# Kernel optimization log

Measured on AMD Instinct MI355X. Metric: run time of the kernel, lower is better.

The kernel has to match this reference:

```python
import jax, jax.numpy as jnp
import numpy as np

B = 16384
D = 64            # bottom_mlp_layers[-1] = embedding_dim
DENSE = 512
HIST = 50         # history length per row
C_CAMP = 1000     # num_collisions for campaign table (sqrt(1e6))
C_FEAT = 316      # num_collisions for 1e5-vocab tables
NQ_CAMP = 1000    # ceil(1e6/1000)
NQ_FEAT = 317     # ceil(1e5/316)
NFEAT = 7
N = NFEAT + 1 + 1 # sparse features + dense row
PROJ = 128


def setup_inputs() -> dict:
    key = jax.random.key(0)
    ks = jax.random.split(key, 20)
    inp = {
        'x': jax.random.normal(ks[0], (B, DENSE), jnp.float32),
        'hist_idx': jax.random.randint(ks[1], (B * HIST,), 0, 1000000),
        'hist_offsets': jnp.arange(B, dtype=jnp.int64) * HIST,
        'feat_idx': jax.random.randint(ks[2], (B, NFEAT), 0, 100000),
        # QR embedding tables (quotient, remainder)
        'Wq_c': jax.random.normal(ks[3], (NQ_CAMP, D), jnp.float32) * 0.05,
        'Wr_c': jax.random.normal(ks[4], (C_CAMP, D), jnp.float32) * 0.05,
        'Wq_f': jax.random.normal(ks[5], (NFEAT, NQ_FEAT, D), jnp.float32) * 0.05,
        'Wr_f': jax.random.normal(ks[6], (NFEAT, C_FEAT, D), jnp.float32) * 0.05,
        # bottom MLP: 512->512 relu 512->256 relu 256->64
        'W0': jax.random.normal(ks[7], (512, DENSE), jnp.float32) * 0.03,
        'b0': jnp.zeros((512,), jnp.float32),
        'W1': jax.random.normal(ks[8], (256, 512), jnp.float32) * 0.04,
        'b1': jnp.zeros((256,), jnp.float32),
        'W2': jax.random.normal(ks[9], (64, 256), jnp.float32) * 0.06,
        'b2': jnp.zeros((64,), jnp.float32),
        # projection: (D + (N^2-N)/2) -> PROJ ; 64 + 36 = 100
        'Wp': jax.random.normal(ks[10], (PROJ, D + (N * N - N) // 2), jnp.float32) * 0.1,
        'bp': jnp.zeros((PROJ,), jnp.float32),
    }
    return inp


def _forward(x, hist_idx, hist_offsets, feat_idx, Wq_c, Wr_c, Wq_f, Wr_f,
             W0, b0, W1, b1, W2, b2, Wp, bp):
    # bottom MLP
    h = jax.nn.relu(x @ W0.T + b0)
    h = jax.nn.relu(h @ W1.T + b1)
    dense = h @ W2.T + b2                                   # [B, D]

    # QR embedding bag (mode='mean', operation='mult') for history feature
    e = Wq_c[hist_idx // C_CAMP] * Wr_c[hist_idx % C_CAMP]  # [M, D]
    M = hist_idx.shape[0]
    seg = jnp.cumsum(jnp.zeros((M,), jnp.int32).at[hist_offsets].add(1)) - 1
    sums = jax.ops.segment_sum(e, seg, num_segments=B)      # [B, D]
    counts = jnp.diff(jnp.concatenate([hist_offsets, jnp.array([M], hist_offsets.dtype)]))
    hist_emb = sums / counts[:, None].astype(sums.dtype)

    # single-valued QR lookups (bag size 1 -> mean == lookup)
    t = jnp.arange(NFEAT)[None, :]
    fe = Wq_f[t, feat_idx // C_FEAT] * Wr_f[t, feat_idx % C_FEAT]  # [B, NFEAT, D]

    # pairwise dot interaction: upper triangle (offset=1) of T @ T^T
    T = jnp.concatenate([dense[:, None, :], hist_emb[:, None, :], fe], axis=1)  # [B, N, D]
    Z = jnp.einsum('bnd,bmd->bnm', T, T)
    row, col = np.triu_indices(N, k=1)
    Z_flat = Z[:, row, col]                                  # [B, (N^2-N)/2]

    combined = jnp.concatenate([dense, Z_flat], axis=1)
    return combined @ Wp.T + bp                              # [B, PROJ]


def reference(x, hist_idx, hist_offsets, feat_idx, Wq_c, Wr_c, Wq_f, Wr_f,
              W0, b0, W1, b1, W2, b2, Wp, bp):
    return _forward(x, hist_idx, hist_offsets, feat_idx, Wq_c, Wr_c, Wq_f, Wr_f,
                    W0, b0, W1, b1, W2, b2, Wp, bp)
```

## Files before the change

### kernel.cpp

```cpp
#include <hip/hip_runtime.h>
#include <hip/hip_bf16.h>
#include <stdint.h>

#define DENSE_D 512
#define HIDDEN1 512
#define HIDDEN2 256
#define EMB_D   64
#define NFEAT   7
#define NROWS   9
#define NPAIRS  36
#define COMB    100
#define KPROJ   128
#define PROJ    128
#define C_CAMP  1000
#define C_FEAT  316
#define NQ_FEAT 317
#define TROWS   16
#define HISTMAX 52

typedef __attribute__((ext_vector_type(8)))  __bf16 bf16x8;
typedef __attribute__((ext_vector_type(8)))  unsigned short ushort8;
typedef __attribute__((ext_vector_type(4)))  float  facc4;

#define GLD_LDS16(gp, lp) __builtin_amdgcn_global_load_lds( \
    (__attribute__((address_space(1))) void*)(gp), \
    (__attribute__((address_space(3))) void*)(lp), 16, 0, 0)

__device__ inline unsigned short f2bf(float f) {
    __hip_bfloat16 h = __float2bfloat16(f);
    return *reinterpret_cast<unsigned short*>(&h);
}
__device__ inline float blo(unsigned int u) { return __uint_as_float(u << 16); }
__device__ inline float bhi(unsigned int u) { return __uint_as_float(u & 0xffff0000u); }

template<int BM, int BN, int BK, int WM, int WN, bool RELU, bool A_F32>
__global__ __launch_bounds__(WM * WN * 64)
void gemm16(const void* __restrict__ Avoid,
            const unsigned short* __restrict__ W,
            const float* __restrict__ bias,
            unsigned short* __restrict__ Cout,
            int M, int N, int K)
{
    constexpr int THREADS = WM * WN * 64;
    constexpr int MREP    = BM / (WM * 16);
    constexpr int NREP    = BN / (WN * 16);
    constexpr int SUB     = BK / 32;
    constexpr int ACH     = BM * BK / 8;
    constexpr int BCH     = BN * BK / 8;

    __shared__ __align__(16) unsigned short Asm[BK / 8][BM][8];
    __shared__ __align__(16) unsigned short Bsm[BK / 8][BN][8];

    const int tid  = threadIdx.x;
    const int lane = tid & 63;
    const int wave = tid >> 6;
    const int wm   = wave / WN;
    const int wn   = wave % WN;
    const int row0 = blockIdx.x * BM;
    const int col0 = blockIdx.y * BN;
    const int fr   = lane & 15;
    const int fk   = lane >> 4;

    facc4 acc[MREP][NREP] = {};

    for (int k0 = 0; k0 < K; k0 += BK) {
        if (A_F32) {
            const float* Af = (const float*)Avoid;
            #pragma unroll
            for (int it = 0; it < ACH / THREADS; ++it) {
                const int p  = it * THREADS + tid;
                const int r  = p & (BM - 1);
                const int kc = p / BM;
                const float* src = Af + (size_t)(row0 + r) * K + k0 + kc * 8;
                const float4 v0 = *reinterpret_cast<const float4*>(src);
                const float4 v1 = *reinterpret_cast<const float4*>(src + 4);
                ushort8 cv;
                cv[0] = f2bf(v0.x); cv[1] = f2bf(v0.y);
                cv[2] = f2bf(v0.z); cv[3] = f2bf(v0.w);
                cv[4] = f2bf(v1.x); cv[5] = f2bf(v1.y);
                cv[6] = f2bf(v1.z); cv[7] = f2bf(v1.w);
                *reinterpret_cast<ushort8*>(
                    (unsigned short*)(&Asm[0][0][0]) + (size_t)p * 8) = cv;
            }
        } else {
            const unsigned short* Ab = (const unsigned short*)Avoid;
            #pragma unroll
            for (int it = 0; it < ACH / THREADS; ++it) {
                const int p  = it * THREADS + tid;
                const int r  = p & (BM - 1);
                const int kc = p / BM;
                GLD_LDS16(Ab + (size_t)(row0 + r) * K + k0 + kc * 8,
                          (&Asm[0][0][0]) + (size_t)p * 8);
            }
        }
        #pragma unroll
        for (int it = 0; it < BCH / THREADS; ++it) {
            const int p  = it * THREADS + tid;
            const int r  = p & (BN - 1);
            const int kc = p / BN;
            GLD_LDS16(W + (size_t)(col0 + r) * K + k0 + kc * 8,
                      (&Bsm[0][0][0]) + (size_t)p * 8);
        }
        __syncthreads();

        #pragma unroll
        for (int s = 0; s < SUB; ++s) {
            bf16x8 af[MREP], bw[NREP];
            #pragma unroll
            for (int m = 0; m < MREP; ++m)
                af[m] = *reinterpret_cast<const bf16x8*>(
                    &Asm[s * 4 + fk][wm * (MREP * 16) + m * 16 + fr][0]);
            #pragma unroll
            for (int n = 0; n < NREP; ++n)
                bw[n] = *reinterpret_cast<const bf16x8*>(
                    &Bsm[s * 4 + fk][wn * (NREP * 16) + n * 16 + fr][0]);
            #pragma unroll
            for (int m = 0; m < MREP; ++m)
                #pragma unroll
                for (int n = 0; n < NREP; ++n)
                    acc[m][n] = __builtin_amdgcn_mfma_f32_16x16x32_bf16(
                        af[m], bw[n], acc[m][n], 0, 0, 0);
        }
        __syncthreads();
    }

    #pragma unroll
    for (int n = 0; n < NREP; ++n) {
        const int col = col0 + wn * (NREP * 16) + n * 16 + fr;
        const float bv = bias[col];
        #pragma unroll
        for (int m = 0; m < MREP; ++m) {
            #pragma unroll
            for (int j = 0; j < 4; ++j) {
                const int row = row0 + wm * (MREP * 16) + m * 16 + fk * 4 + j;
                float v = acc[m][n][j] + bv;
                if (RELU) v = fmaxf(v, 0.f);
                Cout[(size_t)row * N + col] = f2bf(v);
            }
        }
    }
}

__device__ inline void cast_seg(const float* __restrict__ src,
                                unsigned short* __restrict__ dst,
                                int n4, int id, int stride)
{
    for (int i = id; i < n4; i += stride) {
        const float4 v = reinterpret_cast<const float4*>(src)[i];
        ushort4 o;
        o.x = f2bf(v.x); o.y = f2bf(v.y); o.z = f2bf(v.z); o.w = f2bf(v.w);
        reinterpret_cast<ushort4*>(dst)[i] = o;
    }
}

__global__ __launch_bounds__(256)
void prep_all(const float* __restrict__ W0, const float* __restrict__ W1,
              const float* __restrict__ W2, const float* __restrict__ Wp,
              const float* __restrict__ Wq_c, const float* __restrict__ Wr_c,
              const float* __restrict__ Wq_f, const float* __restrict__ Wr_f,
              unsigned short* w0b, unsigned short* w1b, unsigned short* w2b,
              unsigned short* wpb, unsigned short* qcb, unsigned short* rcb,
              unsigned short* qfb, unsigned short* rfb)
{
    const int id = blockIdx.x * blockDim.x + threadIdx.x;
    const int stride = gridDim.x * blockDim.x;
    cast_seg(W0,   w0b, HIDDEN1 * DENSE_D / 4,   id, stride);
    cast_seg(W1,   w1b, HIDDEN2 * HIDDEN1 / 4,   id, stride);
    cast_seg(W2,   w2b, EMB_D * HIDDEN2 / 4,     id, stride);
    cast_seg(Wq_c, qcb, C_CAMP * EMB_D / 4,      id, stride);
    cast_seg(Wr_c, rcb, C_CAMP * EMB_D / 4,      id, stride);
    cast_seg(Wq_f, qfb, NFEAT * NQ_FEAT * EMB_D / 4, id, stride);
    cast_seg(Wr_f, rfb, NFEAT * C_FEAT * EMB_D / 4,  id, stride);
    for (int i = id; i < PROJ * KPROJ; i += stride) {
        const int r = i >> 7, c = i & 127;
        wpb[i] = (c < COMB) ? f2bf(Wp[r * COMB + c]) : (unsigned short)0;
    }
}

__global__ __launch_bounds__(256)
void tail_fused(const unsigned short* __restrict__ h1b,
                const unsigned short* __restrict__ w2b,
                const float* __restrict__ b2,
                const int* __restrict__ hist_idx,
                const int* __restrict__ hist_off,
                const int* __restrict__ feat_idx,
                const unsigned short* __restrict__ qcb,
                const unsigned short* __restrict__ rcb,
                const unsigned short* __restrict__ qfb,
                const unsigned short* __restrict__ rfb,
                const unsigned short* __restrict__ wpb,
                const float* __restrict__ bp,
                float* __restrict__ out,
                int B, int Mtot)
{
    const int r0   = blockIdx.x * TROWS;
    const int t    = threadIdx.x;
    const int lane = t & 63;
    const int wave = t >> 6;
    const int fr   = lane & 15;
    const int fk   = lane >> 4;

    __shared__ __align__(16) unsigned short T[TROWS][NROWS][68];
    __shared__ __align__(16) unsigned short combs[TROWS][136];
    __shared__ int2 soff[TROWS][HISTMAX];

    {
        facc4 acc = {};
        const unsigned short* arow = h1b + (size_t)(r0 + fr) * HIDDEN2;
        const unsigned short* brow = w2b + (size_t)(wave * 16 + fr) * HIDDEN2;
        #pragma unroll
        for (int kw = 0; kw < 8; ++kw) {
            const bf16x8 af = *reinterpret_cast<const bf16x8*>(arow + kw * 32 + fk * 8);
            const bf16x8 bw = *reinterpret_cast<const bf16x8*>(brow + kw * 32 + fk * 8);
            acc = __builtin_amdgcn_mfma_f32_16x16x32_bf16(af, bw, acc, 0, 0, 0);
        }
        const int col = wave * 16 + fr;
        const float bv = b2[col];
        #pragma unroll
        for (int j = 0; j < 4; ++j) {
            const int row = fk * 4 + j;
            const unsigned short hv = f2bf(acc[j] + bv);
            T[row][0][col]  = hv;
            combs[row][col] = hv;
        }
    }

    for (int p = t; p < TROWS * 18; p += 256) {
        const int row = p / 18, c = p % 18;
        *reinterpret_cast<unsigned int*>(&combs[row][100 + c * 2]) = 0u;
    }

    {
        const int row = t >> 4;
        const int oc  = t & 15;
        const int br  = r0 + row;

        const int fbase = br * NFEAT;
        #pragma unroll
        for (int f = 0; f < NFEAT; ++f) {
            const int fi = feat_idx[fbase + f];
            const int q = fi / C_FEAT, r = fi - q * C_FEAT;
            const uint2 qv = *reinterpret_cast<const uint2*>(
                qfb + ((size_t)f * NQ_FEAT + q) * EMB_D + oc * 4);
            const uint2 rv = *reinterpret_cast<const uint2*>(
                rfb + ((size_t)f * C_FEAT + r) * EMB_D + oc * 4);
            union { ushort4 v; uint2 u; } pk;
            pk.v.x = f2bf(blo(qv.x) * blo(rv.x));
            pk.v.y = f2bf(bhi(qv.x) * bhi(rv.x));
            pk.v.z = f2bf(blo(qv.y) * blo(rv.y));
            pk.v.w = f2bf(bhi(qv.y) * bhi(rv.y));
            *reinterpret_cast<uint2*>(&T[row][2 + f][oc * 4]) = pk.u;
        }

        const int start = hist_off[br];
        const int end   = (br + 1 < B) ? hist_off[br + 1] : Mtot;
        const int cnt   = end - start;
        const int* hp = hist_idx + start;
        for (int i = oc; i < cnt; i += 16) {
            const int hi = hp[i];
            const int q = hi / C_CAMP;
            soff[row][i] = make_int2(q * EMB_D, (hi - q * C_CAMP) * EMB_D);
        }

        const unsigned short* qb = qcb + oc * 4;
        const unsigned short* rb = rcb + oc * 4;
        float a0 = 0.f, a1 = 0.f, a2 = 0.f, a3 = 0.f;
        #pragma unroll 2
        for (int i = 0; i < cnt; ++i) {
            const int2 o = soff[row][i];
            const uint2 qv = *reinterpret_cast<const uint2*>(qb + o.x);
            const uint2 rv = *reinterpret_cast<const uint2*>(rb + o.y);
            a0 += blo(qv.x) * blo(rv.x);
            a1 += bhi(qv.x) * bhi(rv.x);
            a2 += blo(qv.y) * blo(rv.y);
            a3 += bhi(qv.y) * bhi(rv.y);
        }
        const float inv = 1.f / (float)max(cnt, 1);
        union { ushort4 v; uint2 u; } pk;
        pk.v.x = f2bf(a0 * inv); pk.v.y = f2bf(a1 * inv);
        pk.v.z = f2bf(a2 * inv); pk.v.w = f2bf(a3 * inv);
        *reinterpret_cast<uint2*>(&T[row][1][oc * 4]) = pk.u;
    }
    __syncthreads();

    for (int p = t; p < NPAIRS * TROWS; p += 256) {
        const int row = p & (TROWS - 1);
        const int pr  = p / TROWS;
        int i = 0, rem = pr;
        while (rem >= (NROWS - 1) - i) { rem -= (NROWS - 1) - i; ++i; }
        const int j = i + 1 + rem;
        const unsigned short* ti = &T[row][i][0];
        const unsigned short* tj = &T[row][j][0];
        float s = 0.f;
        #pragma unroll
        for (int d = 0; d < EMB_D; d += 4) {
            const uint2 u = *reinterpret_cast<const uint2*>(ti + d);
            const uint2 v = *reinterpret_cast<const uint2*>(tj + d);
            s += blo(u.x) * blo(v.x) + bhi(u.x) * bhi(v.x)
               + blo(u.y) * blo(v.y) + bhi(u.y) * bhi(v.y);
        }
        combs[row][EMB_D + pr] = f2bf(s);
    }
    __syncthreads();

    {
        facc4 acc[2] = {};
        #pragma unroll
        for (int kw = 0; kw < 4; ++kw) {
            const bf16x8 af = *reinterpret_cast<const bf16x8*>(
                &combs[fr][kw * 32 + fk * 8]);
            #pragma unroll
            for (int n = 0; n < 2; ++n) {
                const bf16x8 bw = *reinterpret_cast<const bf16x8*>(
                    wpb + (size_t)(wave * 32 + n * 16 + fr) * KPROJ + kw * 32 + fk * 8);
                acc[n] = __builtin_amdgcn_mfma_f32_16x16x32_bf16(af, bw, acc[n], 0, 0, 0);
            }
        }
        #pragma unroll
        for (int n = 0; n < 2; ++n) {
            const int col = wave * 32 + n * 16 + fr;
            const float bv = bp[col];
            #pragma unroll
            for (int j = 0; j < 4; ++j) {
                const int row = fk * 4 + j;
                out[(size_t)(r0 + row) * PROJ + col] = acc[n][j] + bv;
            }
        }
    }
}

extern "C" void kernel_launch(void* const* d_in, const int* in_sizes, int n_in,
                              void* d_out, int out_size, void* d_ws, size_t ws_size,
                              hipStream_t stream)
{
    const float* x        = (const float*)d_in[0];
    const int*   hist_idx = (const int*)  d_in[1];
    const int*   hist_off = (const int*)  d_in[2];
    const int*   feat_idx = (const int*)  d_in[3];
    const float* Wq_c     = (const float*)d_in[4];
    const float* Wr_c     = (const float*)d_in[5];
    const float* Wq_f     = (const float*)d_in[6];
    const float* Wr_f     = (const float*)d_in[7];
    const float* W0       = (const float*)d_in[8];
    const float* b0       = (const float*)d_in[9];
    const float* W1       = (const float*)d_in[10];
    const float* b1       = (const float*)d_in[11];
    const float* W2       = (const float*)d_in[12];
    const float* b2       = (const float*)d_in[13];
    const float* Wp       = (const float*)d_in[14];
    const float* bp       = (const float*)d_in[15];

    const int M    = in_sizes[0] / DENSE_D;
    const int Mtot = in_sizes[1];

    char* w = (char*)d_ws;
    auto take = [&](size_t bytes) { char* p = w; w += (bytes + 255) & ~(size_t)255; return p; };
    unsigned short* w0b = (unsigned short*)take(HIDDEN1 * DENSE_D * 2);
    unsigned short* w1b = (unsigned short*)take(HIDDEN2 * HIDDEN1 * 2);
    unsigned short* w2b = (unsigned short*)take(EMB_D * HIDDEN2 * 2);
    unsigned short* wpb = (unsigned short*)take(PROJ * KPROJ * 2);
    unsigned short* qcb = (unsigned short*)take(C_CAMP * EMB_D * 2);
    unsigned short* rcb = (unsigned short*)take(C_CAMP * EMB_D * 2);
    unsigned short* qfb = (unsigned short*)take(NFEAT * NQ_FEAT * EMB_D * 2);
    unsigned short* rfb = (unsigned short*)take(NFEAT * C_FEAT * EMB_D * 2);
    unsigned short* h0b = (unsigned short*)take((size_t)M * HIDDEN1 * 2);
    unsigned short* h1b = (unsigned short*)take((size_t)M * HIDDEN2 * 2);

    prep_all<<<256, 256, 0, stream>>>(W0, W1, W2, Wp, Wq_c, Wr_c, Wq_f, Wr_f,
                                      w0b, w1b, w2b, wpb, qcb, rcb, qfb, rfb);

    gemm16<128, 128, 32, 2, 2, true, true>
        <<<dim3(M / 128, HIDDEN1 / 128), 256, 0, stream>>>(
        x, w0b, b0, h0b, M, HIDDEN1, DENSE_D);

    gemm16<64, 128, 64, 1, 4, true, false>
        <<<dim3(M / 64, HIDDEN2 / 128), 256, 0, stream>>>(
        h0b, w1b, b1, h1b, M, HIDDEN2, HIDDEN1);

    tail_fused<<<M / TROWS, 256, 0, stream>>>(
        h1b, w2b, b2, hist_idx, hist_off, feat_idx,
        qcb, rcb, qfb, rfb, wpb, bp, (float*)d_out, M, Mtot);
}
```

Before: 85.07 us.

## Drop weight-cast prep kernel; cast weights on the fly and widen tail kernel

Removes the separate prep_all kernel that converted all weights and embedding tables to bf16. The GEMMs now load fp32 weights and convert them during tiling, and the first GEMM also casts the campaign QR tables as a side task. The tail kernel reads fp32 W2, Wp and the feature tables directly. It also grows to 512 threads and splits the history-bag gather across two halves, whose partial sums are reduced through shared memory. This saves one launch and a pass over the weights, at the cost of repeated fp32 loads and conversions in every block and direct LDS stores in place of async global_load_lds for B tiles.

Result: slower. 104.0 us (+22.2%).

```diff
diff --git a/kernel.cpp b/kernel.cpp
--- a/kernel.cpp
+++ b/kernel.cpp
@@ -10,7 +10,6 @@
 #define NROWS   9
 #define NPAIRS  36
 #define COMB    100
-#define KPROJ   128
 #define PROJ    128
 #define C_CAMP  1000
 #define C_FEAT  316
@@ -33,13 +32,18 @@
 __device__ inline float blo(unsigned int u) { return __uint_as_float(u << 16); }
 __device__ inline float bhi(unsigned int u) { return __uint_as_float(u & 0xffff0000u); }
 
-template<int BM, int BN, int BK, int WM, int WN, bool RELU, bool A_F32>
+union bfr8 { bf16x8 v; ushort8 u; };
+
+template<int BM, int BN, int BK, int WM, int WN, bool RELU,
+         bool A_F32, bool B_F32, bool CAST>
 __global__ __launch_bounds__(WM * WN * 64)
 void gemm16(const void* __restrict__ Avoid,
-            const unsigned short* __restrict__ W,
+            const void* __restrict__ Wvoid,
             const float* __restrict__ bias,
             unsigned short* __restrict__ Cout,
-            int M, int N, int K)
+            int M, int N, int K,
+            const float* __restrict__ qc, const float* __restrict__ rc,
+            unsigned short* __restrict__ qcb, unsigned short* __restrict__ rcb)
 {
     constexpr int THREADS = WM * WN * 64;
     constexpr int MREP    = BM / (WM * 16);
@@ -60,6 +64,19 @@
     const int col0 = blockIdx.y * BN;
     const int fr   = lane & 15;
     const int fk   = lane >> 4;
+
+    if (CAST) {
+        constexpr int N4 = C_CAMP * EMB_D / 4;
+        const int gid = (blockIdx.y * gridDim.x + blockIdx.x) * THREADS + tid;
+        if (gid < 2 * N4) {
+            const bool second = gid >= N4;
+            const int i = second ? gid - N4 : gid;
+            const float4 v = reinterpret_cast<const float4*>(second ? rc : qc)[i];
+            ushort4 o;
+            o.x = f2bf(v.x); o.y = f2bf(v.y); o.z = f2bf(v.z); o.w = f2bf(v.w);
+            reinterpret_cast<ushort4*>(second ? rcb : qcb)[i] = o;
+        }
+    }
 
     facc4 acc[MREP][NREP] = {};
 
@@ -93,13 +110,34 @@
                           (&Asm[0][0][0]) + (size_t)p * 8);
             }
         }
-        #pragma unroll
-        for (int it = 0; it < BCH / THREADS; ++it) {
-            const int p  = it * THREADS + tid;
-            const int r  = p & (BN - 1);
-            const int kc = p / BN;
-            GLD_LDS16(W + (size_t)(col0 + r) * K + k0 + kc * 8,
-                      (&Bsm[0][0][0]) + (size_t)p * 8);
+        if (B_F32) {
+            const float* Wf = (const float*)Wvoid;
+            #pragma unroll
+            for (int it = 0; it < BCH / THREADS; ++it) {
+                const int p  = it * THREADS + tid;
+                const int r  = p & (BN - 1);
+                const int kc = p / BN;
+                const float* src = Wf + (size_t)(col0 + r) * K + k0 + kc * 8;
+                const float4 v0 = *reinterpret_cast<const float4*>(src);
+                const float4 v1 = *reinterpret_cast<const float4*>(src + 4);
+                ushort8 cv;
+                cv[0] = f2bf(v0.x); cv[1] = f2bf(v0.y);
+                cv[2] = f2bf(v0.z); cv[3] = f2bf(v0.w);
+                cv[4] = f2bf(v1.x); cv[5] = f2bf(v1.y);
+                cv[6] = f2bf(v1.z); cv[7] = f2bf(v1.w);
+                *reinterpret_cast<ushort8*>(
+                    (unsigned short*)(&Bsm[0][0][0]) + (size_t)p * 8) = cv;
+            }
+        } else {
+            const unsigned short* Wb = (const unsigned short*)Wvoid;
+            #pragma unroll
+            for (int it = 0; it < BCH / THREADS; ++it) {
+                const int p  = it * THREADS + tid;
+                const int r  = p & (BN - 1);
+                const int kc = p / BN;
+                GLD_LDS16(Wb + (size_t)(col0 + r) * K + k0 + kc * 8,
+                          (&Bsm[0][0][0]) + (size_t)p * 8);
+            }
         }
         __syncthreads();
 
@@ -141,54 +179,18 @@
     }
 }
 
-__device__ inline void cast_seg(const float* __restrict__ src,
-                                unsigned short* __restrict__ dst,
-                                int n4, int id, int stride)
-{
-    for (int i = id; i < n4; i += stride) {
-        const float4 v = reinterpret_cast<const float4*>(src)[i];
-        ushort4 o;
-        o.x = f2bf(v.x); o.y = f2bf(v.y); o.z = f2bf(v.z); o.w = f2bf(v.w);
-        reinterpret_cast<ushort4*>(dst)[i] = o;
-    }
-}
-
-__global__ __launch_bounds__(256)
-void prep_all(const float* __restrict__ W0, const float* __restrict__ W1,
-              const float* __restrict__ W2, const float* __restrict__ Wp,
-              const float* __restrict__ Wq_c, const float* __restrict__ Wr_c,
-              const float* __restrict__ Wq_f, const float* __restrict__ Wr_f,
-              unsigned short* w0b, unsigned short* w1b, unsigned short* w2b,
-              unsigned short* wpb, unsigned short* qcb, unsigned short* rcb,
-              unsigned short* qfb, unsigned short* rfb)
-{
-    const int id = blockIdx.x * blockDim.x + threadIdx.x;
-    const int stride = gridDim.x * blockDim.x;
-    cast_seg(W0,   w0b, HIDDEN1 * DENSE_D / 4,   id, stride);
-    cast_seg(W1,   w1b, HIDDEN2 * HIDDEN1 / 4,   id, stride);
-    cast_seg(W2,   w2b, EMB_D * HIDDEN2 / 4,     id, stride);
-    cast_seg(Wq_c, qcb, C_CAMP * EMB_D / 4,      id, stride);
-    cast_seg(Wr_c, rcb, C_CAMP * EMB_D / 4,      id, stride);
-    cast_seg(Wq_f, qfb, NFEAT * NQ_FEAT * EMB_D / 4, id, stride);
-    cast_seg(Wr_f, rfb, NFEAT * C_FEAT * EMB_D / 4,  id, stride);
-    for (int i = id; i < PROJ * KPROJ; i += stride) {
-        const int r = i >> 7, c = i & 127;
-        wpb[i] = (c < COMB) ? f2bf(Wp[r * COMB + c]) : (unsigned short)0;
-    }
-}
-
-__global__ __launch_bounds__(256)
+__global__ __launch_bounds__(512)
 void tail_fused(const unsigned short* __restrict__ h1b,
-                const unsigned short* __restrict__ w2b,
+                const float* __restrict__ W2,
                 const float* __restrict__ b2,
                 const int* __restrict__ hist_idx,
                 const int* __restrict__ hist_off,
                 const int* __restrict__ feat_idx,
                 const unsigned short* __restrict__ qcb,
                 const unsigned short* __restrict__ rcb,
-                const unsigned short* __restrict__ qfb,
-                const unsigned short* __restrict__ rfb,
-                const unsigned short* __restrict__ wpb,
+                const float* __restrict__ Wq_f,
+                const float* __restrict__ Wr_f,
+                const float* __restrict__ Wp,
                 const float* __restrict__ bp,
                 float* __restrict__ out,
                 int B, int Mtot)
@@ -202,17 +204,24 @@
 
     __shared__ __align__(16) unsigned short T[TROWS][NROWS][68];
     __shared__ __align__(16) unsigned short combs[TROWS][136];
-    __shared__ int2 soff[TROWS][HISTMAX];
-
-    {
+    __shared__ int2  soff[TROWS][HISTMAX];
+    __shared__ float part[TROWS][68];
+
+    if (wave < 4) {
         facc4 acc = {};
         const unsigned short* arow = h1b + (size_t)(r0 + fr) * HIDDEN2;
-        const unsigned short* brow = w2b + (size_t)(wave * 16 + fr) * HIDDEN2;
+        const float* brow = W2 + (size_t)(wave * 16 + fr) * HIDDEN2;
         #pragma unroll
         for (int kw = 0; kw < 8; ++kw) {
             const bf16x8 af = *reinterpret_cast<const bf16x8*>(arow + kw * 32 + fk * 8);
-            const bf16x8 bw = *reinterpret_cast<const bf16x8*>(brow + kw * 32 + fk * 8);
-            acc = __builtin_amdgcn_mfma_f32_16x16x32_bf16(af, bw, acc, 0, 0, 0);
+            const float4 w0 = *reinterpret_cast<const float4*>(brow + kw * 32 + fk * 8);
+            const float4 w1 = *reinterpret_cast<const float4*>(brow + kw * 32 + fk * 8 + 4);
+            bfr8 bw;
+            bw.u[0] = f2bf(w0.x); bw.u[1] = f2bf(w0.y);
+            bw.u[2] = f2bf(w0.z); bw.u[3] = f2bf(w0.w);
+            bw.u[4] = f2bf(w1.x); bw.u[5] = f2bf(w1.y);
+            bw.u[6] = f2bf(w1.z); bw.u[7] = f2bf(w1.w);
+            acc = __builtin_amdgcn_mfma_f32_16x16x32_bf16(af, bw.v, acc, 0, 0, 0);
         }
         const int col = wave * 16 + fr;
         const float bv = b2[col];
@@ -225,30 +234,30 @@
         }
     }
 
-    for (int p = t; p < TROWS * 18; p += 256) {
+    for (int p = t; p < TROWS * 18; p += 512) {
         const int row = p / 18, c = p % 18;
         *reinterpret_cast<unsigned int*>(&combs[row][100 + c * 2]) = 0u;
     }
 
     {
-        const int row = t >> 4;
-        const int oc  = t & 15;
-        const int br  = r0 + row;
+        const int row  = (t >> 4) & 15;
+        const int oc   = t & 15;
+        const int half = t >> 8;
+        const int br   = r0 + row;
 
         const int fbase = br * NFEAT;
-        #pragma unroll
-        for (int f = 0; f < NFEAT; ++f) {
+        for (int f = half ? 4 : 0; f < (half ? NFEAT : 4); ++f) {
             const int fi = feat_idx[fbase + f];
             const int q = fi / C_FEAT, r = fi - q * C_FEAT;
-            const uint2 qv = *reinterpret_cast<const uint2*>(
-                qfb + ((size_t)f * NQ_FEAT + q) * EMB_D + oc * 4);
-            const uint2 rv = *reinterpret_cast<const uint2*>(
-                rfb + ((size_t)f * C_FEAT + r) * EMB_D + oc * 4);
+            const float4 qv = *reinterpret_cast<const float4*>(
+                Wq_f + ((size_t)f * NQ_FEAT + q) * EMB_D + oc * 4);
+            const float4 rv = *reinterpret_cast<const float4*>(
+                Wr_f + ((size_t)f * C_FEAT + r) * EMB_D + oc * 4);
             union { ushort4 v; uint2 u; } pk;
-            pk.v.x = f2bf(blo(qv.x) * blo(rv.x));
-            pk.v.y = f2bf(bhi(qv.x) * bhi(rv.x));
-            pk.v.z = f2bf(blo(qv.y) * blo(rv.y));
-            pk.v.w = f2bf(bhi(qv.y) * bhi(rv.y));
+            pk.v.x = f2bf(qv.x * rv.x);
+            pk.v.y = f2bf(qv.y * rv.y);
+            pk.v.z = f2bf(qv.z * rv.z);
+            pk.v.w = f2bf(qv.w * rv.w);
             *reinterpret_cast<uint2*>(&T[row][2 + f][oc * 4]) = pk.u;
         }
 
@@ -256,7 +265,7 @@
         const int end   = (br + 1 < B) ? hist_off[br + 1] : Mtot;
         const int cnt   = end - start;
         const int* hp = hist_idx + start;
-        for (int i = oc; i < cnt; i += 16) {
+        for (int i = half + 2 * oc; i < cnt; i += 32) {
             const int hi = hp[i];
             const int q = hi / C_CAMP;
             soff[row][i] = make_int2(q * EMB_D, (hi - q * C_CAMP) * EMB_D);
@@ -266,7 +275,7 @@
         const unsigned short* rb = rcb + oc * 4;
         float a0 = 0.f, a1 = 0.f, a2 = 0.f, a3 = 0.f;
         #pragma unroll 2
-        for (int i = 0; i < cnt; ++i) {
+        for (int i = half; i < cnt; i += 2) {
             const int2 o = soff[row][i];
             const uint2 qv = *reinterpret_cast<const uint2*>(qb + o.x);
             const uint2 rv = *reinterpret_cast<const uint2*>(rb + o.y);
@@ -275,15 +284,24 @@
             a2 += blo(qv.y) * blo(rv.y);
             a3 += bhi(qv.y) * bhi(rv.y);
         }
-        const float inv = 1.f / (float)max(cnt, 1);
-        union { ushort4 v; uint2 u; } pk;
-        pk.v.x = f2bf(a0 * inv); pk.v.y = f2bf(a1 * inv);
-        pk.v.z = f2bf(a2 * inv); pk.v.w = f2bf(a3 * inv);
-        *reinterpret_cast<uint2*>(&T[row][1][oc * 4]) = pk.u;
+        if (half == 1) {
+            part[row][oc * 4 + 0] = a0; part[row][oc * 4 + 1] = a1;
+            part[row][oc * 4 + 2] = a2; part[row][oc * 4 + 3] = a3;
+        }
+        __syncthreads();
+        if (half == 0) {
+            const float inv = 1.f / (float)max(cnt, 1);
+            union { ushort4 v; uint2 u; } pk;
+            pk.v.x = f2bf((a0 + part[row][oc * 4 + 0]) * inv);
+            pk.v.y = f2bf((a1 + part[row][oc * 4 + 1]) * inv);
+            pk.v.z = f2bf((a2 + part[row][oc * 4 + 2]) * inv);
+            pk.v.w = f2bf((a3 + part[row][oc * 4 + 3]) * inv);
+            *reinterpret_cast<uint2*>(&T[row][1][oc * 4]) = pk.u;
+        }
     }
     __syncthreads();
 
-    for (int p = t; p < NPAIRS * TROWS; p += 256) {
+    for (int p = t; p < NPAIRS * TROWS; p += 512) {
         const int row = p & (TROWS - 1);
         const int pr  = p / TROWS;
         int i = 0, rem = pr;
@@ -303,17 +321,41 @@
     }
     __syncthreads();
 
-    {
+    if (wave < 4) {
         facc4 acc[2] = {};
         #pragma unroll
-        for (int kw = 0; kw < 4; ++kw) {
+        for (int kw = 0; kw < 3; ++kw) {
             const bf16x8 af = *reinterpret_cast<const bf16x8*>(
                 &combs[fr][kw * 32 + fk * 8]);
             #pragma unroll
             for (int n = 0; n < 2; ++n) {
-                const bf16x8 bw = *reinterpret_cast<const bf16x8*>(
-                    wpb + (size_t)(wave * 32 + n * 16 + fr) * KPROJ + kw * 32 + fk * 8);
-                acc[n] = __builtin_amdgcn_mfma_f32_16x16x32_bf16(af, bw, acc[n], 0, 0, 0);
+                const int col = wave * 32 + n * 16 + fr;
+                const float* wrow = Wp + (size_t)col * COMB + kw * 32 + fk * 8;
+                const float4 w0 = *reinterpret_cast<const float4*>(wrow);
+                const float4 w1 = *reinterpret_cast<const float4*>(wrow + 4);
+                bfr8 bw;
+                bw.u[0] = f2bf(w0.x); bw.u[1] = f2bf(w0.y);
+                bw.u[2] = f2bf(w0.z); bw.u[3] = f2bf(w0.w);
+                bw.u[4] = f2bf(w1.x); bw.u[5] = f2bf(w1.y);
+                bw.u[6] = f2bf(w1.z); bw.u[7] = f2bf(w1.w);
+                acc[n] = __builtin_amdgcn_mfma_f32_16x16x32_bf16(af, bw.v, acc[n], 0, 0, 0);
+            }
+        }
+        {
+            const bf16x8 af = *reinterpret_cast<const bf16x8*>(&combs[fr][96 + fk * 8]);
+            #pragma unroll
+            for (int n = 0; n < 2; ++n) {
+                const int col = wave * 32 + n * 16 + fr;
+                bfr8 bw;
+                #pragma unroll
+                for (int j = 0; j < 8; ++j) bw.u[j] = 0;
+                if (fk == 0) {
+                    const float4 w0 = *reinterpret_cast<const float4*>(
+                        Wp + (size_t)col * COMB + 96);
+                    bw.u[0] = f2bf(w0.x); bw.u[1] = f2bf(w0.y);
+                    bw.u[2] = f2bf(w0.z); bw.u[3] = f2bf(w0.w);
+                }
+                acc[n] = __builtin_amdgcn_mfma_f32_16x16x32_bf16(af, bw.v, acc[n], 0, 0, 0);
             }
         }
         #pragma unroll
@@ -355,29 +397,20 @@
 
     char* w = (char*)d_ws;
     auto take = [&](size_t bytes) { char* p = w; w += (bytes + 255) & ~(size_t)255; return p; };
-    unsigned short* w0b = (unsigned short*)take(HIDDEN1 * DENSE_D * 2);
-    unsigned short* w1b = (unsigned short*)take(HIDDEN2 * HIDDEN1 * 2);
-    unsigned short* w2b = (unsigned short*)take(EMB_D * HIDDEN2 * 2);
-    unsigned short* wpb = (unsigned short*)take(PROJ * KPROJ * 2);
+    unsigned short* h0b = (unsigned short*)take((size_t)M * HIDDEN1 * 2);
+    unsigned short* h1b = (unsigned short*)take((size_t)M * HIDDEN2 * 2);
     unsigned short* qcb = (unsigned short*)take(C_CAMP * EMB_D * 2);
     unsigned short* rcb = (unsigned short*)take(C_CAMP * EMB_D * 2);
-    unsigned short* qfb = (unsigned short*)take(NFEAT * NQ_FEAT * EMB_D * 2);
-    unsigned short* rfb = (unsigned short*)take(NFEAT * C_FEAT * EMB_D * 2);
-    unsigned short* h0b = (unsigned short*)take((size_t)M * HIDDEN1 * 2);
-    unsigned short* h1b = (unsigned short*)take((size_t)M * HIDDEN2 * 2);
-
-    prep_all<<<256, 256, 0, stream>>>(W0, W1, W2, Wp, Wq_c, Wr_c, Wq_f, Wr_f,
-                                      w0b, w1b, w2b, wpb, qcb, rcb, qfb, rfb);
-
-    gemm16<128, 128, 32, 2, 2, true, true>
+
+    gemm16<128, 128, 32, 2, 2, true, true, true, true>
         <<<dim3(M / 128, HIDDEN1 / 128), 256, 0, stream>>>(
-        x, w0b, b0, h0b, M, HIDDEN1, DENSE_D);
-
-    gemm16<64, 128, 64, 1, 4, true, false>
+        x, W0, b0, h0b, M, HIDDEN1, DENSE_D, Wq_c, Wr_c, qcb, rcb);
+
+    gemm16<64, 128, 64, 1, 4, true, false, true, false>
         <<<dim3(M / 64, HIDDEN2 / 128), 256, 0, stream>>>(
-        h0b, w1b, b1, h1b, M, HIDDEN2, HIDDEN1);
-
-    tail_fused<<<M / TROWS, 256, 0, stream>>>(
-        h1b, w2b, b2, hist_idx, hist_off, feat_idx,
-        qcb, rcb, qfb, rfb, wpb, bp, (float*)d_out, M, Mtot);
+        h0b, W1, b1, h1b, M, HIDDEN2, HIDDEN1, nullptr, nullptr, nullptr, nullptr);
+
+    tail_fused<<<M / TROWS, 512, 0, stream>>>(
+        h1b, W2, b2, hist_idx, hist_off, feat_idx,
+        qcb, rcb, Wq_f, Wr_f, Wp, bp, (float*)d_out, M, Mtot);
 }
```

## Use one wave per row in tail kernel with shuffle-based history gather

Applied to the files above, without the earlier changes.

The tail kernel grows from 256 to 1024 threads per block, so each of the 16 rows gets a full wave instead of 16 threads. History indices are decoded once per lane and broadcast with shuffles, which removes the LDS offset table. Each wave half then processes alternate bag entries with 4-byte coalesced loads, and the halves are combined with an xor shuffle. The MLP and projection stages now use only a subset of waves, so some waves sit idle there, and the larger blocks may reduce occupancy flexibility.

After: 88.52 us. 4.0% more time.

```diff
diff --git a/kernel.cpp b/kernel.cpp
--- a/kernel.cpp
+++ b/kernel.cpp
@@ -16,7 +16,6 @@
 #define C_FEAT  316
 #define NQ_FEAT 317
 #define TROWS   16
-#define HISTMAX 52
 
 typedef __attribute__((ext_vector_type(8)))  __bf16 bf16x8;
 typedef __attribute__((ext_vector_type(8)))  unsigned short ushort8;
@@ -32,6 +31,9 @@
 }
 __device__ inline float blo(unsigned int u) { return __uint_as_float(u << 16); }
 __device__ inline float bhi(unsigned int u) { return __uint_as_float(u & 0xffff0000u); }
+__device__ inline unsigned int pack2(unsigned short lo, unsigned short hi) {
+    return (unsigned int)lo | ((unsigned int)hi << 16);
+}
 
 template<int BM, int BN, int BK, int WM, int WN, bool RELU, bool A_F32>
 __global__ __launch_bounds__(WM * WN * 64)
@@ -177,7 +179,7 @@
     }
 }
 
-__global__ __launch_bounds__(256)
+__global__ __launch_bounds__(1024)
 void tail_fused(const unsigned short* __restrict__ h1b,
                 const unsigned short* __restrict__ w2b,
                 const float* __restrict__ b2,
@@ -202,9 +204,8 @@
 
     __shared__ __align__(16) unsigned short T[TROWS][NROWS][68];
     __shared__ __align__(16) unsigned short combs[TROWS][136];
-    __shared__ int2 soff[TROWS][HISTMAX];
-
-    {
+
+    if (wave < 4) {
         facc4 acc = {};
         const unsigned short* arow = h1b + (size_t)(r0 + fr) * HIDDEN2;
         const unsigned short* brow = w2b + (size_t)(wave * 16 + fr) * HIDDEN2;
@@ -225,65 +226,69 @@
         }
     }
 
-    for (int p = t; p < TROWS * 18; p += 256) {
+    for (int p = t; p < TROWS * 18; p += 1024) {
         const int row = p / 18, c = p % 18;
         *reinterpret_cast<unsigned int*>(&combs[row][100 + c * 2]) = 0u;
     }
 
     {
-        const int row = t >> 4;
-        const int oc  = t & 15;
+        const int row = wave;
         const int br  = r0 + row;
-
-        const int fbase = br * NFEAT;
-        #pragma unroll
-        for (int f = 0; f < NFEAT; ++f) {
-            const int fi = feat_idx[fbase + f];
-            const int q = fi / C_FEAT, r = fi - q * C_FEAT;
-            const uint2 qv = *reinterpret_cast<const uint2*>(
-                qfb + ((size_t)f * NQ_FEAT + q) * EMB_D + oc * 4);
-            const uint2 rv = *reinterpret_cast<const uint2*>(
-                rfb + ((size_t)f * C_FEAT + r) * EMB_D + oc * 4);
-            union { ushort4 v; uint2 u; } pk;
-            pk.v.x = f2bf(blo(qv.x) * blo(rv.x));
-            pk.v.y = f2bf(bhi(qv.x) * bhi(rv.x));
-            pk.v.z = f2bf(blo(qv.y) * blo(rv.y));
-            pk.v.w = f2bf(bhi(qv.y) * bhi(rv.y));
-            *reinterpret_cast<uint2*>(&T[row][2 + f][oc * 4]) = pk.u;
+        const int h   = lane >> 5;
+        const int l2  = lane & 31;
+
+        #pragma unroll
+        for (int j = 0; j < 4; ++j) {
+            const int f = h * 4 + j;
+            if (f < NFEAT) {
+                const int fi = feat_idx[br * NFEAT + f];
+                const int q = fi / C_FEAT, r = fi - q * C_FEAT;
+                const unsigned int qv = *reinterpret_cast<const unsigned int*>(
+                    qfb + ((size_t)f * NQ_FEAT + q) * EMB_D + 2 * l2);
+                const unsigned int rv = *reinterpret_cast<const unsigned int*>(
+                    rfb + ((size_t)f * C_FEAT + r) * EMB_D + 2 * l2);
+                *reinterpret_cast<unsigned int*>(&T[row][2 + f][2 * l2]) =
+                    pack2(f2bf(blo(qv) * blo(rv)), f2bf(bhi(qv) * bhi(rv)));
+            }
         }
 
         const int start = hist_off[br];
         const int end   = (br + 1 < B) ? hist_off[br + 1] : Mtot;
         const int cnt   = end - start;
-        const int* hp = hist_idx + start;
-        for (int i = oc; i < cnt; i += 16) {
-            const int hi = hp[i];
-            const int q = hi / C_CAMP;
-            soff[row][i] = make_int2(q * EMB_D, (hi - q * C_CAMP) * EMB_D);
-        }
-
-        const unsigned short* qb = qcb + oc * 4;
-        const unsigned short* rb = rcb + oc * 4;
-        float a0 = 0.f, a1 = 0.f, a2 = 0.f, a3 = 0.f;
-        #pragma unroll 2
-        for (int i = 0; i < cnt; ++i) {
-            const int2 o = soff[row][i];
-            const uint2 qv = *reinterpret_cast<const uint2*>(qb + o.x);
-            const uint2 rv = *reinterpret_cast<const uint2*>(rb + o.y);
-            a0 += blo(qv.x) * blo(rv.x);
-            a1 += bhi(qv.x) * bhi(rv.x);
-            a2 += blo(qv.y) * blo(rv.y);
-            a3 += bhi(qv.y) * bhi(rv.y);
-        }
-        const float inv = 1.f / (float)max(cnt, 1);
-        union { ushort4 v; uint2 u; } pk;
-        pk.v.x = f2bf(a0 * inv); pk.v.y = f2bf(a1 * inv);
-        pk.v.z = f2bf(a2 * inv); pk.v.w = f2bf(a3 * inv);
-        *reinterpret_cast<uint2*>(&T[row][1][oc * 4]) = pk.u;
+        int qo = 0, ro = 0;
+        if (lane < cnt) {
+            const int hi = hist_idx[start + lane];
+            const int qq = hi / C_CAMP;
+            qo = qq * EMB_D;
+            ro = (hi - qq * C_CAMP) * EMB_D;
+        }
+
+        float a0 = 0.f, a1 = 0.f;
+        const int nit = (cnt + 1) >> 1;
+        for (int i = 0; i < nit; ++i) {
+            const int idx = 2 * i + h;
+            const int qoi = __shfl(qo, idx);
+            const int roi = __shfl(ro, idx);
+            const unsigned int uq = *reinterpret_cast<const unsigned int*>(
+                qcb + qoi + 2 * l2);
+            const unsigned int ur = *reinterpret_cast<const unsigned int*>(
+                rcb + roi + 2 * l2);
+            if (idx < cnt) {
+                a0 += blo(uq) * blo(ur);
+                a1 += bhi(uq) * bhi(ur);
+            }
+        }
+        a0 += __shfl_xor(a0, 32);
+        a1 += __shfl_xor(a1, 32);
+        if (h == 0) {
+            const float inv = 1.f / (float)max(cnt, 1);
+            *reinterpret_cast<unsigned int*>(&T[row][1][2 * l2]) =
+                pack2(f2bf(a0 * inv), f2bf(a1 * inv));
+        }
     }
     __syncthreads();
 
-    for (int p = t; p < NPAIRS * TROWS; p += 256) {
+    for (int p = t; p < NPAIRS * TROWS; p += 1024) {
         const int row = p & (TROWS - 1);
         const int pr  = p / TROWS;
         int i = 0, rem = pr;
@@ -303,28 +308,22 @@
     }
     __syncthreads();
 
-    {
-        facc4 acc[2] = {};
+    if (wave < 8) {
+        facc4 acc = {};
         #pragma unroll
         for (int kw = 0; kw < 4; ++kw) {
             const bf16x8 af = *reinterpret_cast<const bf16x8*>(
                 &combs[fr][kw * 32 + fk * 8]);
-            #pragma unroll
-            for (int n = 0; n < 2; ++n) {
-                const bf16x8 bw = *reinterpret_cast<const bf16x8*>(
-                    wpb + (size_t)(wave * 32 + n * 16 + fr) * KPROJ + kw * 32 + fk * 8);
-                acc[n] = __builtin_amdgcn_mfma_f32_16x16x32_bf16(af, bw, acc[n], 0, 0, 0);
-            }
-        }
-        #pragma unroll
-        for (int n = 0; n < 2; ++n) {
-            const int col = wave * 32 + n * 16 + fr;
-            const float bv = bp[col];
-            #pragma unroll
-            for (int j = 0; j < 4; ++j) {
-                const int row = fk * 4 + j;
-                out[(size_t)(r0 + row) * PROJ + col] = acc[n][j] + bv;
-            }
+            const bf16x8 bw = *reinterpret_cast<const bf16x8*>(
+                wpb + (size_t)(wave * 16 + fr) * KPROJ + kw * 32 + fk * 8);
+            acc = __builtin_amdgcn_mfma_f32_16x16x32_bf16(af, bw, acc, 0, 0, 0);
+        }
+        const int col = wave * 16 + fr;
+        const float bv = bp[col];
+        #pragma unroll
+        for (int j = 0; j < 4; ++j) {
+            const int row = fk * 4 + j;
+            out[(size_t)(r0 + row) * PROJ + col] = acc[j] + bv;
         }
     }
 }
@@ -377,7 +376,7 @@
         <<<dim3(M / 64, HIDDEN2 / 128), 256, 0, stream>>>(
         h0b, w1b, b1, h1b, M, HIDDEN2, HIDDEN1);
 
-    tail_fused<<<M / TROWS, 256, 0, stream>>>(
+    tail_fused<<<M / TROWS, 1024, 0, stream>>>(
         h1b, w2b, b2, hist_idx, hist_off, feat_idx,
         qcb, rcb, qfb, rfb, wpb, bp, (float*)d_out, M, Mtot);
 }
```

## Split history embedding-bag gather into separate kernel with wider loads

Applied to the files above, without the earlier changes.

Moves the QR history embedding-bag mean out of the fused tail kernel into a dedicated hist_gather kernel that runs before the MLP GEMMs. It writes a bf16 per-row embedding to workspace. The new kernel uses 16-byte loads, splits each bag across 4 slots with shuffle reductions, and unrolls by 4 for more memory parallelism. The tail kernel then just copies the precomputed row. This adds a kernel launch and an extra workspace round-trip, and assumes at most 64 history entries per row.

Result: faster. 82.31 us, median of 3 (-3.2%).

```diff
diff --git a/kernel.cpp b/kernel.cpp
--- a/kernel.cpp
+++ b/kernel.cpp
@@ -16,7 +16,8 @@
 #define C_FEAT  316
 #define NQ_FEAT 317
 #define TROWS   16
-#define HISTMAX 52
+#define GROWS   8
+#define HISTMAX 64
 
 typedef __attribute__((ext_vector_type(8)))  __bf16 bf16x8;
 typedef __attribute__((ext_vector_type(8)))  unsigned short ushort8;
@@ -178,20 +179,112 @@
 }
 
 __global__ __launch_bounds__(256)
-void tail_fused(const unsigned short* __restrict__ h1b,
-                const unsigned short* __restrict__ w2b,
-                const float* __restrict__ b2,
-                const int* __restrict__ hist_idx,
-                const int* __restrict__ hist_off,
-                const int* __restrict__ feat_idx,
-                const unsigned short* __restrict__ qcb,
-                const unsigned short* __restrict__ rcb,
-                const unsigned short* __restrict__ qfb,
-                const unsigned short* __restrict__ rfb,
-                const unsigned short* __restrict__ wpb,
-                const float* __restrict__ bp,
-                float* __restrict__ out,
-                int B, int Mtot)
+void hist_gather(const int* __restrict__ hist_idx,
+                 const int* __restrict__ hist_off,
+                 const unsigned short* __restrict__ qcb,
+                 const unsigned short* __restrict__ rcb,
+                 unsigned short* __restrict__ hemb,
+                 int B, int Mtot)
+{
+    const int r0 = blockIdx.x * GROWS;
+    const int t  = threadIdx.x;
+
+    __shared__ int2 soff[GROWS][HISTMAX];
+    __shared__ int  scnt[GROWS];
+
+    for (int p = t; p < GROWS * HISTMAX; p += 256) {
+        const int row = p >> 6;
+        const int i   = p & 63;
+        const int br  = r0 + row;
+        const int start = hist_off[br];
+        const int end   = (br + 1 < B) ? hist_off[br + 1] : Mtot;
+        const int cnt   = end - start;
+        int2 o = make_int2(0, 0);
+        if (i < cnt) {
+            const int hi = hist_idx[start + i];
+            const int q = hi / C_CAMP;
+            o = make_int2(q * EMB_D, (hi - q * C_CAMP) * EMB_D);
+        }
+        soff[row][i] = o;
+        if (i == 0) scnt[row] = cnt;
+    }
+    __syncthreads();
+
+    const int lane = t & 63;
+    const int wv   = t >> 6;
+    const int half = lane >> 5;
+    const int row  = wv * 2 + half;
+    const int l5   = lane & 31;
+    const int slot = l5 >> 3;
+    const int d8   = l5 & 7;
+    const int cnt  = scnt[row];
+
+    const unsigned short* qb = qcb + d8 * 8;
+    const unsigned short* rb = rcb + d8 * 8;
+
+    float a[8] = {};
+    #define ACC8(q, r) do { \
+        a[0] += blo((q).x) * blo((r).x); a[1] += bhi((q).x) * bhi((r).x); \
+        a[2] += blo((q).y) * blo((r).y); a[3] += bhi((q).y) * bhi((r).y); \
+        a[4] += blo((q).z) * blo((r).z); a[5] += bhi((q).z) * bhi((r).z); \
+        a[6] += blo((q).w) * blo((r).w); a[7] += bhi((q).w) * bhi((r).w); } while (0)
+
+    const int full = cnt >> 2;
+    int g = 0;
+    for (; g + 4 <= full; g += 4) {
+        int2 o[4];
+        #pragma unroll
+        for (int j = 0; j < 4; ++j) o[j] = soff[row][(g + j) * 4 + slot];
+        uint4 uq[4], ur[4];
+        #pragma unroll
+        for (int j = 0; j < 4; ++j) {
+            uq[j] = *reinterpret_cast<const uint4*>(qb + o[j].x);
+            ur[j] = *reinterpret_cast<const uint4*>(rb + o[j].y);
+        }
+        #pragma unroll
+        for (int j = 0; j < 4; ++j) ACC8(uq[j], ur[j]);
+    }
+    for (; g < full; ++g) {
+        const int2 o = soff[row][g * 4 + slot];
+        const uint4 uq = *reinterpret_cast<const uint4*>(qb + o.x);
+        const uint4 ur = *reinterpret_cast<const uint4*>(rb + o.y);
+        ACC8(uq, ur);
+    }
+    {
+        const int idx = (full << 2) + slot;
+        const int2 o = soff[row][idx & (HISTMAX - 1)];
+        const uint4 uq = *reinterpret_cast<const uint4*>(qb + o.x);
+        const uint4 ur = *reinterpret_cast<const uint4*>(rb + o.y);
+        if (idx < cnt) ACC8(uq, ur);
+    }
+    #undef ACC8
+
+    #pragma unroll
+    for (int k = 0; k < 8; ++k) {
+        a[k] += __shfl_xor(a[k], 8);
+        a[k] += __shfl_xor(a[k], 16);
+    }
+
+    if (slot == 0) {
+        const float inv = 1.f / (float)max(cnt, 1);
+        union { unsigned short s[8]; uint4 u; } pk;
+        #pragma unroll
+        for (int k = 0; k < 8; ++k) pk.s[k] = f2bf(a[k] * inv);
+        *reinterpret_cast<uint4*>(hemb + (size_t)(r0 + row) * EMB_D + d8 * 8) = pk.u;
+    }
+}
+
+__global__ __launch_bounds__(256)
+void tail_rest(const unsigned short* __restrict__ h1b,
+               const unsigned short* __restrict__ w2b,
+               const float* __restrict__ b2,
+               const unsigned short* __restrict__ hemb,
+               const int* __restrict__ feat_idx,
+               const unsigned short* __restrict__ qfb,
+               const unsigned short* __restrict__ rfb,
+               const unsigned short* __restrict__ wpb,
+               const float* __restrict__ bp,
+               float* __restrict__ out)
 {
     const int r0   = blockIdx.x * TROWS;
     const int t    = threadIdx.x;
@@ -200,9 +293,8 @@
     const int fr   = lane & 15;
     const int fk   = lane >> 4;
 
-    __shared__ __align__(16) unsigned short T[TROWS][NROWS][68];
+    __shared__ __align__(16) unsigned short T[TROWS][NROWS][72];
     __shared__ __align__(16) unsigned short combs[TROWS][136];
-    __shared__ int2 soff[TROWS][HISTMAX];
 
     {
         facc4 acc = {};
@@ -230,11 +322,17 @@
         *reinterpret_cast<unsigned int*>(&combs[row][100 + c * 2]) = 0u;
     }
 
+    if (t < TROWS * 8) {
+        const int row = t >> 3, o8 = t & 7;
+        const uint4 v = *reinterpret_cast<const uint4*>(
+            hemb + (size_t)(r0 + row) * EMB_D + o8 * 8);
+        *reinterpret_cast<uint4*>(&T[row][1][o8 * 8]) = v;
+    }
+
     {
         const int row = t >> 4;
         const int oc  = t & 15;
         const int br  = r0 + row;
-
         const int fbase = br * NFEAT;
         #pragma unroll
         for (int f = 0; f < NFEAT; ++f) {
@@ -251,35 +349,6 @@
             pk.v.w = f2bf(bhi(qv.y) * bhi(rv.y));
             *reinterpret_cast<uint2*>(&T[row][2 + f][oc * 4]) = pk.u;
         }
-
-        const int start = hist_off[br];
-        const int end   = (br + 1 < B) ? hist_off[br + 1] : Mtot;
-        const int cnt   = end - start;
-        const int* hp = hist_idx + start;
-        for (int i = oc; i < cnt; i += 16) {
-            const int hi = hp[i];
-            const int q = hi / C_CAMP;
-            soff[row][i] = make_int2(q * EMB_D, (hi - q * C_CAMP) * EMB_D);
-        }
-
-        const unsigned short* qb = qcb + oc * 4;
-        const unsigned short* rb = rcb + oc * 4;
-        float a0 = 0.f, a1 = 0.f, a2 = 0.f, a3 = 0.f;
-        #pragma unroll 2
-        for (int i = 0; i < cnt; ++i) {
-            const int2 o = soff[row][i];
-            const uint2 qv = *reinterpret_cast<const uint2*>(qb + o.x);
-            const uint2 rv = *reinterpret_cast<const uint2*>(rb + o.y);
-            a0 += blo(qv.x) * blo(rv.x);
-            a1 += bhi(qv.x) * bhi(rv.x);
-            a2 += blo(qv.y) * blo(rv.y);
-            a3 += bhi(qv.y) * bhi(rv.y);
-        }
-        const float inv = 1.f / (float)max(cnt, 1);
-        union { ushort4 v; uint2 u; } pk;
-        pk.v.x = f2bf(a0 * inv); pk.v.y = f2bf(a1 * inv);
-        pk.v.z = f2bf(a2 * inv); pk.v.w = f2bf(a3 * inv);
-        *reinterpret_cast<uint2*>(&T[row][1][oc * 4]) = pk.u;
     }
     __syncthreads();
 
@@ -365,9 +434,13 @@
     unsigned short* rfb = (unsigned short*)take(NFEAT * C_FEAT * EMB_D * 2);
     unsigned short* h0b = (unsigned short*)take((size_t)M * HIDDEN1 * 2);
     unsigned short* h1b = (unsigned short*)take((size_t)M * HIDDEN2 * 2);
+    unsigned short* hem = (unsigned short*)take((size_t)M * EMB_D * 2);
 
     prep_all<<<256, 256, 0, stream>>>(W0, W1, W2, Wp, Wq_c, Wr_c, Wq_f, Wr_f,
                                       w0b, w1b, w2b, wpb, qcb, rcb, qfb, rfb);
+
+    hist_gather<<<M / GROWS, 256, 0, stream>>>(
+        hist_idx, hist_off, qcb, rcb, hem, M, Mtot);
 
     gemm16<128, 128, 32, 2, 2, true, true>
         <<<dim3(M / 128, HIDDEN1 / 128), 256, 0, stream>>>(
@@ -377,7 +450,6 @@
         <<<dim3(M / 64, HIDDEN2 / 128), 256, 0, stream>>>(
         h0b, w1b, b1, h1b, M, HIDDEN2, HIDDEN1);
 
-    tail_fused<<<M / TROWS, 256, 0, stream>>>(
-        h1b, w2b, b2, hist_idx, hist_off, feat_idx,
-        qcb, rcb, qfb, rfb, wpb, bp, (float*)d_out, M, Mtot);
-}
+    tail_rest<<<M / TROWS, 256, 0, stream>>>(
+        h1b, w2b, b2, hem, feat_idx, qfb, rfb, wpb, bp, (float*)d_out);
+}
```
